# Optimization experiments

Hardware: AMD Instinct MI355X
Metric: run time of the kernel (lower is better)

## Reference

```python
import jax, jax.numpy as jnp
import numpy as np
import math

B, S, DM, H = 2, 2048, 1024, 16
DH = DM // H  # 64


def setup_inputs() -> dict:
    key = jax.random.key(0)
    ks = jax.random.split(key, 12)
    s = 1.0 / math.sqrt(DM)
    inp = {
        "key": jax.random.normal(ks[0], (B, S, DM), jnp.float32),
        "value": jax.random.normal(ks[1], (B, S, DM), jnp.float32),
        "query": jax.random.normal(ks[2], (B, S, DM), jnp.float32),
        # causal mask: True = masked out (matches masked_fill semantics)
        "mask": jnp.broadcast_to(~jnp.tril(jnp.ones((S, S), bool)), (B, S, S)),
        "Wk": jax.random.normal(ks[3], (DM, DM), jnp.float32) * s,
        "bk": jnp.zeros((DM,), jnp.float32),
        "Wv": jax.random.normal(ks[4], (DM, DM), jnp.float32) * s,
        "bv": jnp.zeros((DM,), jnp.float32),
        "Wq": jax.random.normal(ks[5], (DM, DM), jnp.float32) * s,
        "bq": jnp.zeros((DM,), jnp.float32),
        "Wo": jax.random.normal(ks[6], (DM, DM), jnp.float32) * s,
        "bo": jnp.zeros((DM,), jnp.float32),
    }
    return inp


def _split_heads(x):
    # [B, S, H*DH] -> [B, H, S, DH]
    b, s, _ = x.shape
    return x.reshape(b, s, H, DH).transpose(0, 2, 1, 3)


def reference(key, value, query, mask, Wk, bk, Wv, bv, Wq, bq, Wo, bo):
    key_up = _split_heads(key @ Wk.T + bk)      # [B,H,S,DH]
    value_up = _split_heads(value @ Wv.T + bv)  # [B,H,S,DH]
    query_up = _split_heads(query @ Wq.T + bq) / math.sqrt(DH)
    scores = jnp.einsum("bhqd,bhkd->bhqk", query_up, key_up)  # [B,H,S,S]
    scores = jnp.where(mask[:, None, :, :], jnp.float32(-1e18), scores)
    attn = jax.nn.softmax(scores, axis=-1)
    # dropout is identity in eval mode
    context = jnp.einsum("bhqk,bhkd->bhqd", attn, value_up)
    context = context.transpose(0, 2, 1, 3).reshape(key.shape[0], -1, H * DH)
    output = context @ Wo.T + bo                # [B,S,DM]
    top_attn = attn[:, 0, :, :]                 # [B,S,S]
    return output, top_attn
```

## Files before the change

kernel.cpp:

```cpp
#include <hip/hip_runtime.h>
#include <hip/hip_bf16.h>
#include <math.h>

#define B_ 2
#define S_ 2048
#define DM_ 1024
#define H_ 16
#define DH_ 64

using short8 = __attribute__((ext_vector_type(8))) short;
using f32x4  = __attribute__((ext_vector_type(4))) float;

typedef const __attribute__((address_space(1))) void* gas_cvp;
typedef __attribute__((address_space(3))) void* las_vp;

struct CvtJobs {
    const float* in[7];
    ushort* out[7];
    int n[7];
};

__device__ __forceinline__ ushort f2bu(float x) {
    __hip_bfloat16 h = __float2bfloat16(x);
    return *(ushort*)&h;
}

__global__ __launch_bounds__(256) void cvt_bf16(CvtJobs jobs) {
    const int j = blockIdx.y;
    const int n = jobs.n[j];
    const int idx = (blockIdx.x * 256 + threadIdx.x) * 8;
    if (idx >= n) return;
    const float* in = jobs.in[j];
    float4 a = *(const float4*)&in[idx];
    float4 b = *(const float4*)&in[idx + 4];
    ushort u[8];
    u[0] = f2bu(a.x); u[1] = f2bu(a.y); u[2] = f2bu(a.z); u[3] = f2bu(a.w);
    u[4] = f2bu(b.x); u[5] = f2bu(b.y); u[6] = f2bu(b.z); u[7] = f2bu(b.w);
    *(int4*)&jobs.out[j][idx] = *(int4*)u;
}

#define GEMM_STAGE(buf, k0v)                                                   \
    {                                                                          \
        _Pragma("unroll")                                                      \
        for (int i = 0; i < 2; i++) {                                          \
            const int s   = i * 256 + tid;                                     \
            const int c   = s >> 7;                                            \
            const int row = s & 127;                                           \
            __builtin_amdgcn_global_load_lds(                                  \
                (gas_cvp)(Ag + (size_t)(i0 + row) * 1024 + (k0v) + c * 8),     \
                (las_vp)&AsB[buf][0][(i * 256 + w * 64) * 8], 16, 0, 0);       \
            __builtin_amdgcn_global_load_lds(                                  \
                (gas_cvp)(Wg + (size_t)(j0 + row) * 1024 + (k0v) + c * 8),     \
                (las_vp)&AsB[buf][1][(i * 256 + w * 64) * 8], 16, 0, 0);       \
        }                                                                      \
    }

struct ProjJobs {
    const ushort* A[3];
    const ushort* W[3];
    const float* bias[3];
    ushort* C[3];
    float scale[3];
};

__global__ __launch_bounds__(256) void gemm_proj3(ProjJobs jobs)
{
    __shared__ ushort AsB[2][2][4096];

    const int o   = blockIdx.x;
    const int swz = (o & 7) * 96 + (o >> 3);
    const int z   = swz >> 8;
    const int rem = swz & 255;
    const int by  = rem >> 3;
    const int bx  = rem & 7;

    const ushort* Ag = jobs.A[z];
    const ushort* Wg = jobs.W[z];
    const float* bias = jobs.bias[z];
    ushort* C = jobs.C[z];
    const float scale = jobs.scale[z];

    const int tid  = threadIdx.x;
    const int w    = tid >> 6;
    const int lane = tid & 63;
    const int g    = lane >> 4;
    const int lr   = lane & 15;
    const int wm   = w >> 1;
    const int wn   = w & 1;
    const int i0   = by * 128;
    const int j0   = bx * 128;

    f32x4 acc[4][4];
    #pragma unroll
    for (int m = 0; m < 4; m++)
        #pragma unroll
        for (int n = 0; n < 4; n++)
            #pragma unroll
            for (int jj = 0; jj < 4; jj++) acc[m][n][jj] = 0.f;

    int cur = 0;
    GEMM_STAGE(0, 0);
    __syncthreads();

    for (int k0 = 0; k0 < 1024; k0 += 32) {
        if (k0 + 32 < 1024) GEMM_STAGE(cur ^ 1, k0 + 32);

        short8 af[4], bf[4];
        #pragma unroll
        for (int m = 0; m < 4; m++)
            af[m] = *(const short8*)&AsB[cur][0][((g << 7) + wm * 64 + m * 16 + lr) * 8];
        #pragma unroll
        for (int n = 0; n < 4; n++)
            bf[n] = *(const short8*)&AsB[cur][1][((g << 7) + wn * 64 + n * 16 + lr) * 8];
        #pragma unroll
        for (int m = 0; m < 4; m++)
            #pragma unroll
            for (int n = 0; n < 4; n++)
                acc[m][n] = __builtin_amdgcn_mfma_f32_16x16x32_bf16(
                    af[m], bf[n], acc[m][n], 0, 0, 0);

        __syncthreads();
        cur ^= 1;
    }

    const int colbase = j0 + wn * 64;
    const int rowbase = i0 + wm * 64;
    #pragma unroll
    for (int n = 0; n < 4; n++) {
        const int col = colbase + n * 16 + lr;
        const float bb = bias[col];
        const int hh = col >> 6;
        const int d = col & 63;
        #pragma unroll
        for (int m = 0; m < 4; m++) {
            const int rb = rowbase + m * 16 + g * 4;
            #pragma unroll
            for (int jj = 0; jj < 4; jj++) {
                const float v = (acc[m][n][jj] + bb) * scale;
                const int i = rb + jj;
                const int b = i >> 11;
                const int srow = i & 2047;
                C[(((size_t)b * H_ + hh) * S_ + srow) * DH_ + d] = f2bu(v);
            }
        }
    }
}

__global__ __launch_bounds__(256) void flash_mfma(
    const ushort* __restrict__ Qb, const ushort* __restrict__ Kb,
    const ushort* __restrict__ Vb, __hip_bfloat16* __restrict__ ctx,
    float* __restrict__ m0, float* __restrict__ l0)
{
    const int p = blockIdx.x;
    const int h = blockIdx.y;
    const int b = blockIdx.z;
    const int qtA = p, qtB = 31 - p;
    const size_t hoff = ((size_t)b * H_ + h) * S_ * DH_;
    const ushort* Qh = Qb + hoff;
    const ushort* Kh = Kb + hoff;
    const ushort* Vh = Vb + hoff;

    __shared__ ushort Ks[64][72];
    __shared__ ushort Vt[64][72];
    __shared__ ushort Ps[4][16][72];

    const int tid  = threadIdx.x;
    const int w    = tid >> 6;
    const int lane = tid & 63;
    const int g    = lane >> 4;
    const int lr   = lane & 15;
    const int q0A  = qtA * 64 + w * 16;
    const int q0B  = qtB * 64 + w * 16;

    short8 qfA0, qfA1, qfB0, qfB1;
    {
        const ushort* qa = Qh + (size_t)(q0A + lr) * DH_ + g * 8;
        qfA0 = *(const short8*)(qa);
        qfA1 = *(const short8*)(qa + 32);
        const ushort* qb = Qh + (size_t)(q0B + lr) * DH_ + g * 8;
        qfB0 = *(const short8*)(qb);
        qfB1 = *(const short8*)(qb + 32);
    }

    f32x4 oA[4], oB[4];
    #pragma unroll
    for (int nc = 0; nc < 4; nc++) {
        oA[nc][0]=0.f; oA[nc][1]=0.f; oA[nc][2]=0.f; oA[nc][3]=0.f;
        oB[nc][0]=0.f; oB[nc][1]=0.f; oB[nc][2]=0.f; oB[nc][3]=0.f;
    }
    float mA = -1e30f, lA = 0.f;
    float mB = -1e30f, lB = 0.f;

    const int nkt = qtB + 1;
    const int c0 = w, c1 = w + 4;

    int4 pk0, pk1, pv0, pv1;
    pk0 = *(const int4*)(Kh + (size_t)lane * DH_ + c0 * 8);
    pk1 = *(const int4*)(Kh + (size_t)lane * DH_ + c1 * 8);
    pv0 = *(const int4*)(Vh + (size_t)lane * DH_ + c0 * 8);
    pv1 = *(const int4*)(Vh + (size_t)lane * DH_ + c1 * 8);

    for (int kt = 0; kt < nkt; kt++) {
        const int kvb = kt * 64;
        __syncthreads();
        {
            *(int4*)&Ks[lane][c0 * 8] = pk0;
            *(int4*)&Ks[lane][c1 * 8] = pk1;
            ushort vv[8];
            *(int4*)vv = pv0;
            #pragma unroll
            for (int j2 = 0; j2 < 8; j2++) Vt[c0 * 8 + j2][lane] = vv[j2];
            *(int4*)vv = pv1;
            #pragma unroll
            for (int j2 = 0; j2 < 8; j2++) Vt[c1 * 8 + j2][lane] = vv[j2];
        }
        if (kt + 1 < nkt) {
            const size_t roff = (size_t)(kvb + 64 + lane) * DH_;
            pk0 = *(const int4*)(Kh + roff + c0 * 8);
            pk1 = *(const int4*)(Kh + roff + c1 * 8);
            pv0 = *(const int4*)(Vh + roff + c0 * 8);
            pv1 = *(const int4*)(Vh + roff + c1 * 8);
        }
        __syncthreads();

        #pragma unroll
        for (int u = 0; u < 2; u++) {
            if (u == 0 && kt > qtA) continue;
            const int qt_u  = (u == 0) ? qtA : qtB;
            const int q0w   = (u == 0) ? q0A : q0B;
            const short8 qf0 = (u == 0) ? qfA0 : qfB0;
            const short8 qf1 = (u == 0) ? qfA1 : qfB1;
            float& m_r = (u == 0) ? mA : mB;
            float& l_r = (u == 0) ? lA : lB;
            f32x4* o   = (u == 0) ? oA : oB;
            const int qglob = q0w + lr;

            f32x4 st[4];
            #pragma unroll
            for (int mt = 0; mt < 4; mt++) { st[mt][0]=0.f; st[mt][1]=0.f; st[mt][2]=0.f; st[mt][3]=0.f; }
            #pragma unroll
            for (int mt = 0; mt < 4; mt++) {
                short8 ka = *(const short8*)&Ks[16 * mt + lr][8 * g];
                short8 kb = *(const short8*)&Ks[16 * mt + lr][32 + 8 * g];
                st[mt] = __builtin_amdgcn_mfma_f32_16x16x32_bf16(ka, qf0, st[mt], 0, 0, 0);
                st[mt] = __builtin_amdgcn_mfma_f32_16x16x32_bf16(kb, qf1, st[mt], 0, 0, 0);
            }

            if (kt == qt_u) {
                #pragma unroll
                for (int mt = 0; mt < 4; mt++)
                    #pragma unroll
                    for (int jj = 0; jj < 4; jj++)
                        if (kvb + 16 * mt + 4 * g + jj > qglob) st[mt][jj] = -1e30f;
            }

            float pmax = st[0][0];
            #pragma unroll
            for (int mt = 0; mt < 4; mt++)
                #pragma unroll
                for (int jj = 0; jj < 4; jj++)
                    pmax = fmaxf(pmax, st[mt][jj]);
            pmax = fmaxf(pmax, __shfl_xor(pmax, 16));
            pmax = fmaxf(pmax, __shfl_xor(pmax, 32));

            const bool defer = __all(pmax - m_r <= 8.0f);
            float mnew = m_r, scv = 1.0f;
            if (!defer) {
                mnew = fmaxf(m_r, pmax);
                scv  = __expf(m_r - mnew);
            }

            float lsum = 0.f;
            #pragma unroll
            for (int mt = 0; mt < 4; mt++)
                #pragma unroll
                for (int jj = 0; jj < 4; jj++) {
                    st[mt][jj] = __expf(st[mt][jj] - mnew);
                    lsum += st[mt][jj];
                }
            lsum += __shfl_xor(lsum, 16);
            lsum += __shfl_xor(lsum, 32);
            l_r = l_r * scv + lsum;
            m_r = mnew;

            if (!defer) {
                float sc0 = __shfl(scv, 4 * g + 0);
                float sc1 = __shfl(scv, 4 * g + 1);
                float sc2 = __shfl(scv, 4 * g + 2);
                float sc3 = __shfl(scv, 4 * g + 3);
                #pragma unroll
                for (int nc = 0; nc < 4; nc++) {
                    o[nc][0] *= sc0; o[nc][1] *= sc1;
                    o[nc][2] *= sc2; o[nc][3] *= sc3;
                }
            }

            #pragma unroll
            for (int mt = 0; mt < 4; mt++) {
                ushort u4[4];
                #pragma unroll
                for (int jj = 0; jj < 4; jj++) u4[jj] = f2bu(st[mt][jj]);
                *(uint2*)&Ps[w][lr][16 * mt + 4 * g] = *(uint2*)u4;
            }

            short8 pa0 = *(const short8*)&Ps[w][lr][8 * g];
            short8 pa1 = *(const short8*)&Ps[w][lr][32 + 8 * g];
            #pragma unroll
            for (int nc = 0; nc < 4; nc++) {
                short8 v0 = *(const short8*)&Vt[16 * nc + lr][8 * g];
                short8 v1 = *(const short8*)&Vt[16 * nc + lr][32 + 8 * g];
                o[nc] = __builtin_amdgcn_mfma_f32_16x16x32_bf16(pa0, v0, o[nc], 0, 0, 0);
                o[nc] = __builtin_amdgcn_mfma_f32_16x16x32_bf16(pa1, v1, o[nc], 0, 0, 0);
            }
        }
    }

    #pragma unroll
    for (int u = 0; u < 2; u++) {
        const int q0w = (u == 0) ? q0A : q0B;
        const float m_r = (u == 0) ? mA : mB;
        const float l_r = (u == 0) ? lA : lB;
        const f32x4* o  = (u == 0) ? oA : oB;
        const float linv = 1.0f / l_r;
        float li0 = __shfl(linv, 4 * g + 0);
        float li1 = __shfl(linv, 4 * g + 1);
        float li2 = __shfl(linv, 4 * g + 2);
        float li3 = __shfl(linv, 4 * g + 3);
        #pragma unroll
        for (int reg = 0; reg < 4; reg++) {
            const int qrow = q0w + 4 * g + reg;
            const float li = (reg == 0) ? li0 : (reg == 1) ? li1 : (reg == 2) ? li2 : li3;
            __hip_bfloat16* cp = ctx + ((size_t)b * S_ + qrow) * DM_ + h * DH_;
            #pragma unroll
            for (int nc = 0; nc < 4; nc++)
                cp[16 * nc + lr] = __float2bfloat16(o[nc][reg] * li);
        }
        if (h == 0 && lane < 16) {
            m0[b * S_ + q0w + lane] = m_r;
            l0[b * S_ + q0w + lane] = l_r;
        }
    }
}

__global__ __launch_bounds__(256) void tail_fused(
    const ushort* __restrict__ ctxb, const ushort* __restrict__ Wg_,
    const float* __restrict__ bo, float* __restrict__ out,
    const ushort* __restrict__ Qb, const ushort* __restrict__ Kb,
    const float* __restrict__ m0, const float* __restrict__ l0,
    float* __restrict__ attn)
{
    __shared__ ushort AsB[2][2][4096];
    const int o = blockIdx.x;
    const int tid = threadIdx.x;
    const int w    = tid >> 6;
    const int lane = tid & 63;
    const int g    = lane >> 4;
    const int lr   = lane & 15;

    if (o < 256) {
        const int swz = (o & 7) * 32 + (o >> 3);
        const int by  = swz >> 3;
        const int bx  = swz & 7;
        const int wm  = w >> 1;
        const int wn  = w & 1;
        const int i0  = by * 128;
        const int j0  = bx * 128;
        const ushort* Ag = ctxb;
        const ushort* Wg = Wg_;

        f32x4 acc[4][4];
        #pragma unroll
        for (int m = 0; m < 4; m++)
            #pragma unroll
            for (int n = 0; n < 4; n++)
                #pragma unroll
                for (int jj = 0; jj < 4; jj++) acc[m][n][jj] = 0.f;

        int cur = 0;
        GEMM_STAGE(0, 0);
        __syncthreads();

        for (int k0 = 0; k0 < 1024; k0 += 32) {
            if (k0 + 32 < 1024) GEMM_STAGE(cur ^ 1, k0 + 32);

            short8 af[4], bf[4];
            #pragma unroll
            for (int m = 0; m < 4; m++)
                af[m] = *(const short8*)&AsB[cur][0][((g << 7) + wm * 64 + m * 16 + lr) * 8];
            #pragma unroll
            for (int n = 0; n < 4; n++)
                bf[n] = *(const short8*)&AsB[cur][1][((g << 7) + wn * 64 + n * 16 + lr) * 8];
            #pragma unroll
            for (int m = 0; m < 4; m++)
                #pragma unroll
                for (int n = 0; n < 4; n++)
                    acc[m][n] = __builtin_amdgcn_mfma_f32_16x16x32_bf16(
                        af[m], bf[n], acc[m][n], 0, 0, 0);

            __syncthreads();
            cur ^= 1;
        }

        const int colbase = j0 + wn * 64;
        const int rowbase = i0 + wm * 64;
        #pragma unroll
        for (int n = 0; n < 4; n++) {
            const int col = colbase + n * 16 + lr;
            const float bb = bo[col];
            #pragma unroll
            for (int m = 0; m < 4; m++) {
                const int rb = rowbase + m * 16 + g * 4;
                #pragma unroll
                for (int jj = 0; jj < 4; jj++)
                    out[(size_t)(rb + jj) * DM_ + col] = acc[m][n][jj] + bb;
            }
        }
        return;
    }

    const int t   = o - 256;
    const int kt  = t & 31;
    const int qt2 = (t >> 5) & 31;
    const int b   = t >> 10;
    float* ap = attn + (size_t)b * S_ * S_;

    if (kt > qt2) {
        const int row = qt2 * 64 + (tid >> 2);
        const int col = kt * 64 + (tid & 3) * 16;
        float4 z = {0.f, 0.f, 0.f, 0.f};
        float* rp = ap + (size_t)row * S_ + col;
        *(float4*)&rp[0]  = z;
        *(float4*)&rp[4]  = z;
        *(float4*)&rp[8]  = z;
        *(float4*)&rp[12] = z;
        return;
    }

    ushort (*Ks)[72] = (ushort(*)[72])&AsB[0][0][0];
    const int q0w = qt2 * 64 + w * 16;
    const int kvb = kt * 64;
    const size_t hoff = (size_t)b * H_ * S_ * DH_;
    const ushort* Qh = Qb + hoff;
    const ushort* Kh = Kb + hoff;

    #pragma unroll
    for (int i = 0; i < 2; i++) {
        const int c = w + 4 * i;
        int4 k4 = *(const int4*)(Kh + (size_t)(kvb + lane) * DH_ + c * 8);
        *(int4*)&Ks[lane][c * 8] = k4;
    }

    short8 qf0, qf1;
    {
        const ushort* qp = Qh + (size_t)(q0w + lr) * DH_ + g * 8;
        qf0 = *(const short8*)(qp);
        qf1 = *(const short8*)(qp + 32);
    }
    const int qglob = q0w + lr;
    const float mv   = m0[b * S_ + qglob];
    const float linv = 1.0f / l0[b * S_ + qglob];
    __syncthreads();

    f32x4 st[4];
    #pragma unroll
    for (int mt = 0; mt < 4; mt++) { st[mt][0]=0.f; st[mt][1]=0.f; st[mt][2]=0.f; st[mt][3]=0.f; }
    #pragma unroll
    for (int mt = 0; mt < 4; mt++) {
        short8 ka = *(const short8*)&Ks[16 * mt + lr][8 * g];
        short8 kb = *(const short8*)&Ks[16 * mt + lr][32 + 8 * g];
        st[mt] = __builtin_amdgcn_mfma_f32_16x16x32_bf16(ka, qf0, st[mt], 0, 0, 0);
        st[mt] = __builtin_amdgcn_mfma_f32_16x16x32_bf16(kb, qf1, st[mt], 0, 0, 0);
    }

    float* rowp = ap + (size_t)qglob * S_ + kvb;
    #pragma unroll
    for (int mt = 0; mt < 4; mt++) {
        float4 ov;
        float v[4];
        #pragma unroll
        for (int jj = 0; jj < 4; jj++) {
            const int kv = 16 * mt + 4 * g + jj;
            float pv = __expf(st[mt][jj] - mv) * linv;
            v[jj] = (kvb + kv > qglob) ? 0.f : pv;
        }
        ov.x = v[0]; ov.y = v[1]; ov.z = v[2]; ov.w = v[3];
        *(float4*)&rowp[16 * mt + 4 * g] = ov;
    }
}

extern "C" void kernel_launch(void* const* d_in, const int* in_sizes, int n_in,
                              void* d_out, int out_size, void* d_ws, size_t ws_size,
                              hipStream_t stream)
{
    const float* key   = (const float*)d_in[0];
    const float* value = (const float*)d_in[1];
    const float* query = (const float*)d_in[2];
    const float* Wk = (const float*)d_in[4];
    const float* bk = (const float*)d_in[5];
    const float* Wv = (const float*)d_in[6];
    const float* bv = (const float*)d_in[7];
    const float* Wq = (const float*)d_in[8];
    const float* bq = (const float*)d_in[9];
    const float* Wo = (const float*)d_in[10];
    const float* bo = (const float*)d_in[11];

    char* ws = (char*)d_ws;
    const size_t per = (size_t)B_ * H_ * S_ * DH_;
    const size_t wsz = (size_t)DM_ * DM_;
    __hip_bfloat16* Qp   = (__hip_bfloat16*)ws;
    __hip_bfloat16* Kp   = Qp + per;
    __hip_bfloat16* Vp   = Kp + per;
    __hip_bfloat16* ctxb = Vp + per;
    __hip_bfloat16* qc   = ctxb + per;
    __hip_bfloat16* kc   = qc + per;
    __hip_bfloat16* vc   = kc + per;
    __hip_bfloat16* wqb  = vc + per;
    __hip_bfloat16* wkb  = wqb + wsz;
    __hip_bfloat16* wvb  = wkb + wsz;
    __hip_bfloat16* wob  = wvb + wsz;
    float* m0 = (float*)(wob + wsz);
    float* l0 = m0 + B_ * S_;

    float* out   = (float*)d_out;
    float* topat = out + (size_t)B_ * S_ * DM_;

    CvtJobs jobs;
    jobs.in[0] = query; jobs.out[0] = (ushort*)qc;  jobs.n[0] = (int)per;
    jobs.in[1] = key;   jobs.out[1] = (ushort*)kc;  jobs.n[1] = (int)per;
    jobs.in[2] = value; jobs.out[2] = (ushort*)vc;  jobs.n[2] = (int)per;
    jobs.in[3] = Wq;    jobs.out[3] = (ushort*)wqb; jobs.n[3] = (int)wsz;
    jobs.in[4] = Wk;    jobs.out[4] = (ushort*)wkb; jobs.n[4] = (int)wsz;
    jobs.in[5] = Wv;    jobs.out[5] = (ushort*)wvb; jobs.n[5] = (int)wsz;
    jobs.in[6] = Wo;    jobs.out[6] = (ushort*)wob; jobs.n[6] = (int)wsz;
    cvt_bf16<<<dim3(2048, 7), 256, 0, stream>>>(jobs);

    ProjJobs pj;
    pj.A[0] = (const ushort*)qc; pj.W[0] = (const ushort*)wqb; pj.bias[0] = bq;
    pj.C[0] = (ushort*)Qp; pj.scale[0] = 0.125f;
    pj.A[1] = (const ushort*)kc; pj.W[1] = (const ushort*)wkb; pj.bias[1] = bk;
    pj.C[1] = (ushort*)Kp; pj.scale[1] = 1.0f;
    pj.A[2] = (const ushort*)vc; pj.W[2] = (const ushort*)wvb; pj.bias[2] = bv;
    pj.C[2] = (ushort*)Vp; pj.scale[2] = 1.0f;
    gemm_proj3<<<768, 256, 0, stream>>>(pj);

    flash_mfma<<<dim3(16, H_, B_), 256, 0, stream>>>(
        (const ushort*)Qp, (const ushort*)Kp, (const ushort*)Vp, ctxb, m0, l0);

    tail_fused<<<256 + B_ * 32 * 32, 256, 0, stream>>>(
        (const ushort*)ctxb, (const ushort*)wob, bo, out,
        (const ushort*)Qp, (const ushort*)Kp, m0, l0, topat);
}
```

Baseline: 157.8 us.

## Triple-buffer GEMM K-loop with vmcnt waits and raise MFMA wave priority

Replaces the double-buffered GEMM main loop in the projection and output GEMMs with a three-stage LDS ring. Loads are issued two stages ahead, and a partial s_waitcnt vmcnt plus a single barrier per iteration replaces the trailing __syncthreads. This is meant to hide global-to-LDS latency better. It also wraps the attention MFMA blocks in s_setprio to favour waves issuing matrix ops. The cost is 50% more LDS per GEMM block (48KB), which may reduce occupancy. Correctness also depends on the exact vmcnt accounting.

```diff
diff --git a/kernel.cpp b/kernel.cpp
--- a/kernel.cpp
+++ b/kernel.cpp
@@ -55,6 +55,38 @@
         }                                                                      \
     }
 
+#define GEMM_KLOOP()                                                           \
+    {                                                                          \
+        int bufc = 0;                                                          \
+        GEMM_STAGE(0, 0);                                                      \
+        GEMM_STAGE(1, 32);                                                     \
+        for (int k0 = 0; k0 < 1024; k0 += 32) {                                \
+            if (k0 + 32 < 1024)                                                \
+                asm volatile("s_waitcnt vmcnt(4)" ::: "memory");               \
+            else                                                               \
+                asm volatile("s_waitcnt vmcnt(0)" ::: "memory");               \
+            __builtin_amdgcn_s_barrier();                                      \
+            if (k0 + 64 < 1024) {                                              \
+                const int nb = (bufc + 2 >= 3) ? bufc - 1 : bufc + 2;          \
+                GEMM_STAGE(nb, k0 + 64);                                       \
+            }                                                                  \
+            short8 af[4], bf[4];                                               \
+            _Pragma("unroll")                                                  \
+            for (int m = 0; m < 4; m++)                                        \
+                af[m] = *(const short8*)&AsB[bufc][0][((g << 7) + wm * 64 + m * 16 + lr) * 8]; \
+            _Pragma("unroll")                                                  \
+            for (int n = 0; n < 4; n++)                                        \
+                bf[n] = *(const short8*)&AsB[bufc][1][((g << 7) + wn * 64 + n * 16 + lr) * 8]; \
+            _Pragma("unroll")                                                  \
+            for (int m = 0; m < 4; m++)                                        \
+                _Pragma("unroll")                                              \
+                for (int n = 0; n < 4; n++)                                    \
+                    acc[m][n] = __builtin_amdgcn_mfma_f32_16x16x32_bf16(       \
+                        af[m], bf[n], acc[m][n], 0, 0, 0);                     \
+            bufc = (bufc + 1 == 3) ? 0 : bufc + 1;                             \
+        }                                                                      \
+    }
+
 struct ProjJobs {
     const ushort* A[3];
     const ushort* W[3];
@@ -65,7 +97,7 @@
 
 __global__ __launch_bounds__(256) void gemm_proj3(ProjJobs jobs)
 {
-    __shared__ ushort AsB[2][2][4096];
+    __shared__ ushort AsB[3][2][4096];
 
     const int o   = blockIdx.x;
     const int swz = (o & 7) * 96 + (o >> 3);
@@ -98,30 +130,7 @@
             #pragma unroll
             for (int jj = 0; jj < 4; jj++) acc[m][n][jj] = 0.f;
 
-    int cur = 0;
-    GEMM_STAGE(0, 0);
-    __syncthreads();
-
-    for (int k0 = 0; k0 < 1024; k0 += 32) {
-        if (k0 + 32 < 1024) GEMM_STAGE(cur ^ 1, k0 + 32);
-
-        short8 af[4], bf[4];
-        #pragma unroll
-        for (int m = 0; m < 4; m++)
-            af[m] = *(const short8*)&AsB[cur][0][((g << 7) + wm * 64 + m * 16 + lr) * 8];
-        #pragma unroll
-        for (int n = 0; n < 4; n++)
-            bf[n] = *(const short8*)&AsB[cur][1][((g << 7) + wn * 64 + n * 16 + lr) * 8];
-        #pragma unroll
-        for (int m = 0; m < 4; m++)
-            #pragma unroll
-            for (int n = 0; n < 4; n++)
-                acc[m][n] = __builtin_amdgcn_mfma_f32_16x16x32_bf16(
-                    af[m], bf[n], acc[m][n], 0, 0, 0);
-
-        __syncthreads();
-        cur ^= 1;
-    }
+    GEMM_KLOOP();
 
     const int colbase = j0 + wn * 64;
     const int rowbase = i0 + wm * 64;
@@ -238,6 +247,7 @@
             f32x4 st[4];
             #pragma unroll
             for (int mt = 0; mt < 4; mt++) { st[mt][0]=0.f; st[mt][1]=0.f; st[mt][2]=0.f; st[mt][3]=0.f; }
+            __builtin_amdgcn_s_setprio(1);
             #pragma unroll
             for (int mt = 0; mt < 4; mt++) {
                 short8 ka = *(const short8*)&Ks[16 * mt + lr][8 * g];
@@ -245,6 +255,7 @@
                 st[mt] = __builtin_amdgcn_mfma_f32_16x16x32_bf16(ka, qf0, st[mt], 0, 0, 0);
                 st[mt] = __builtin_amdgcn_mfma_f32_16x16x32_bf16(kb, qf1, st[mt], 0, 0, 0);
             }
+            __builtin_amdgcn_s_setprio(0);
 
             if (kt == qt_u) {
                 #pragma unroll
@@ -305,6 +316,7 @@
 
             short8 pa0 = *(const short8*)&Ps[w][lr][8 * g];
             short8 pa1 = *(const short8*)&Ps[w][lr][32 + 8 * g];
+            __builtin_amdgcn_s_setprio(1);
             #pragma unroll
             for (int nc = 0; nc < 4; nc++) {
                 short8 v0 = *(const short8*)&Vt[16 * nc + lr][8 * g];
@@ -312,6 +324,7 @@
                 o[nc] = __builtin_amdgcn_mfma_f32_16x16x32_bf16(pa0, v0, o[nc], 0, 0, 0);
                 o[nc] = __builtin_amdgcn_mfma_f32_16x16x32_bf16(pa1, v1, o[nc], 0, 0, 0);
             }
+            __builtin_amdgcn_s_setprio(0);
         }
     }
 
@@ -349,7 +362,7 @@
     const float* __restrict__ m0, const float* __restrict__ l0,
     float* __restrict__ attn)
 {
-    __shared__ ushort AsB[2][2][4096];
+    __shared__ ushort AsB[3][2][4096];
     const int o = blockIdx.x;
     const int tid = threadIdx.x;
     const int w    = tid >> 6;
@@ -376,30 +389,7 @@
                 #pragma unroll
                 for (int jj = 0; jj < 4; jj++) acc[m][n][jj] = 0.f;
 
-        int cur = 0;
-        GEMM_STAGE(0, 0);
-        __syncthreads();
-
-        for (int k0 = 0; k0 < 1024; k0 += 32) {
-            if (k0 + 32 < 1024) GEMM_STAGE(cur ^ 1, k0 + 32);
-
-            short8 af[4], bf[4];
-            #pragma unroll
-            for (int m = 0; m < 4; m++)
-                af[m] = *(const short8*)&AsB[cur][0][((g << 7) + wm * 64 + m * 16 + lr) * 8];
-            #pragma unroll
-            for (int n = 0; n < 4; n++)
-                bf[n] = *(const short8*)&AsB[cur][1][((g << 7) + wn * 64 + n * 16 + lr) * 8];
-            #pragma unroll
-            for (int m = 0; m < 4; m++)
-                #pragma unroll
-                for (int n = 0; n < 4; n++)
-                    acc[m][n] = __builtin_amdgcn_mfma_f32_16x16x32_bf16(
-                        af[m], bf[n], acc[m][n], 0, 0, 0);
-
-            __syncthreads();
-            cur ^= 1;
-        }
+        GEMM_KLOOP();
 
         const int colbase = j0 + wn * 64;
         const int rowbase = i0 + wm * 64;
```

After: 153.7 us. -2.6%, faster.
